# Kernel optimization log

Hardware: AMD Instinct MI355X
Metric: run time of the kernel (lower is better)

## Reference

```python
import jax, jax.numpy as jnp
import numpy as np

NUM_HEADS = 16
D_MODEL = 1024
D_K = D_MODEL // NUM_HEADS


def setup_inputs() -> dict:
    key = jax.random.key(0)
    ks = jax.random.split(key, 11)
    B, S = 2, 2048
    s = 1.0 / np.sqrt(D_MODEL)
    return {
        "Q": jax.random.normal(ks[0], (B, S, D_MODEL), jnp.float32),
        "K": jax.random.normal(ks[1], (B, S, D_MODEL), jnp.float32),
        "V": jax.random.normal(ks[2], (B, S, D_MODEL), jnp.float32),
        "Wq": jax.random.normal(ks[3], (D_MODEL, D_MODEL), jnp.float32) * s,
        "bq": jnp.zeros((D_MODEL,), jnp.float32),
        "Wk": jax.random.normal(ks[4], (D_MODEL, D_MODEL), jnp.float32) * s,
        "bk": jnp.zeros((D_MODEL,), jnp.float32),
        "Wv": jax.random.normal(ks[5], (D_MODEL, D_MODEL), jnp.float32) * s,
        "bv": jnp.zeros((D_MODEL,), jnp.float32),
        "Wo": jax.random.normal(ks[6], (D_MODEL, D_MODEL), jnp.float32) * s,
        "bo": jnp.zeros((D_MODEL,), jnp.float32),
    }


def _split_heads(x):
    B, S, _ = x.shape
    return x.reshape(B, S, NUM_HEADS, D_K).transpose(0, 2, 1, 3)  # (B,H,S,Dk)


def reference(Q, K, V, Wq, bq, Wk, bk, Wv, bv, Wo, bo):
    q = _split_heads(Q @ Wq + bq)
    k = _split_heads(K @ Wk + bk)
    v = _split_heads(V @ Wv + bv)
    scores = jnp.einsum("bhqd,bhkd->bhqk", q, k) / jnp.sqrt(jnp.asarray(D_K, q.dtype))
    attn = jax.nn.softmax(scores, axis=-1)
    out = jnp.einsum("bhqk,bhkd->bhqd", attn, v)  # (B,H,S,Dk)
    B, H, S, Dk = out.shape
    combined = out.transpose(0, 2, 1, 3).reshape(B, S, H * Dk)
    return combined @ Wo + bo
```

## Files before the change

### kernel.cpp

```cpp
#include <hip/hip_runtime.h>
#include <stdint.h>

#define DM   1024
#define NH   16
#define DKH  64
#define SEQ  2048
#define NB   2

typedef __attribute__((ext_vector_type(8))) short  frag8;
typedef __attribute__((ext_vector_type(4))) short  frag4;
typedef __attribute__((ext_vector_type(4))) short  short4v;
typedef __attribute__((ext_vector_type(8))) short  short8v;
typedef __attribute__((ext_vector_type(4))) float  f32x4;

__device__ __forceinline__ unsigned short f2bf(float x){
  unsigned u = __float_as_uint(x);
  u += 0x7fffu + ((u >> 16) & 1u);
  return (unsigned short)(u >> 16);
}

__device__ __forceinline__ float dev_exp2(float x){
  return __builtin_amdgcn_exp2f(x);
}

#define GLOAD16(GP, LP) __builtin_amdgcn_global_load_lds( \
    (__attribute__((address_space(1))) void*)(GP), \
    (__attribute__((address_space(3))) void*)(LP), 16, 0, 0)

#define LDSFENCE() do{ asm volatile("" ::: "memory"); \
                       __builtin_amdgcn_sched_barrier(0); }while(0)



__global__ __launch_bounds__(256) void cast_qkv(const float* __restrict__ Q,
                                                const float* __restrict__ K,
                                                const float* __restrict__ V,
                                                short* __restrict__ dst){
  const int z = blockIdx.z;
  const float* src = (z == 0) ? Q : (z == 1 ? K : V);
  const int i = (blockIdx.x * 256 + threadIdx.x) * 4;
  float4 f = *(const float4*)(src + i);
  short4v s;
  s.x = (short)f2bf(f.x); s.y = (short)f2bf(f.y);
  s.z = (short)f2bf(f.z); s.w = (short)f2bf(f.w);
  *(short4v*)(dst + (long)z * (SEQ*NB*DM) + i) = s;
}

__global__ __launch_bounds__(256) void wtrans(const float* __restrict__ Wq,
                                              const float* __restrict__ Wk,
                                              const float* __restrict__ Wv,
                                              const float* __restrict__ Wo,
                                              short* __restrict__ wt){
  const int z = blockIdx.z;
  const float* W = (z == 0) ? Wq : (z == 1 ? Wk : (z == 2 ? Wv : Wo));
  short* out = wt + (long)z * (DM*DM);
  __shared__ float t[32][33];
  const int n0 = blockIdx.x * 32, k0 = blockIdx.y * 32;
  const int c = threadIdx.x & 31, r0 = threadIdx.x >> 5;
#pragma unroll
  for (int i = 0; i < 4; ++i){
    int r = r0 + i * 8;
    t[r][c] = W[(k0 + r) * DM + n0 + c];
  }
  __syncthreads();
#pragma unroll
  for (int i = 0; i < 4; ++i){
    int r = r0 + i * 8;
    out[(n0 + r) * DM + k0 + c] = (short)f2bf(t[c][r]);
  }
}

__device__ __forceinline__ void store_out(short* p, float v){ *p = (short)f2bf(v); }
__device__ __forceinline__ void store_out(float* p, float v){ *p = v; }

template<typename OT>
__global__ __launch_bounds__(256) void gemm_bt(const short* __restrict__ Abase, long Astride,
                                               const short* __restrict__ Btbase, long Btstride,
                                               const float* __restrict__ bias0,
                                               const float* __restrict__ bias1,
                                               const float* __restrict__ bias2,
                                               OT* __restrict__ Cbase, long Cstride,
                                               float qscale){
  const int z = blockIdx.z;
  const short* A  = Abase + (long)z * Astride;
  const short* Bt = Btbase + (long)z * Btstride;
  OT* C = Cbase + (long)z * Cstride;
  const float* bias = (z == 0) ? bias0 : (z == 1 ? bias1 : bias2);
  const float scale = (z == 0) ? qscale : 1.0f;
  const int KD = DM, ND = DM;

  __shared__ __align__(16) short As[2][128 * 64];
  __shared__ __align__(16) short Bs[2][128 * 64];

  const int tid = threadIdx.x;
  const int w = tid >> 6, lane = tid & 63, l15 = lane & 15, quad = lane >> 4;
  const int wy = w >> 1, wx = w & 1;
  const int bm = blockIdx.x * 128, bn = blockIdx.y * 128;
  const int lrow = lane >> 3;
  const int lcolsw = (((lane & 7) ^ lrow) & 7) * 8;

  f32x4 acc[4][4] = {};

#define GSTAGE(KT, BSEL) do{                                                    \
  _Pragma("unroll")                                                             \
  for (int i_ = 0; i_ < 4; ++i_){                                               \
    int j_ = w * 4 + i_;                                                        \
    GLOAD16(A  + (bm + j_ * 8 + lrow) * KD + (KT) * 64 + lcolsw,                \
            &As[BSEL][j_ * 512]);                                               \
    GLOAD16(Bt + (bn + j_ * 8 + lrow) * KD + (KT) * 64 + lcolsw,                \
            &Bs[BSEL][j_ * 512]);                                               \
  } }while(0)

#define GCOMPUTE(BS) do{                                                        \
  _Pragma("unroll") for (int ks = 0; ks < 2; ++ks){                             \
    frag8 af[4], bf_[4];                                                        \
    _Pragma("unroll") for (int mt = 0; mt < 4; ++mt)                            \
      af[mt] = *(const frag8*)&As[BS][(wy * 64 + mt * 16 + l15) * 64 +          \
                                      (((ks * 4 + quad) ^ (l15 & 7)) * 8)];     \
    _Pragma("unroll") for (int nt = 0; nt < 4; ++nt)                            \
      bf_[nt] = *(const frag8*)&Bs[BS][(wx * 64 + nt * 16 + l15) * 64 +         \
                                       (((ks * 4 + quad) ^ (l15 & 7)) * 8)];    \
    _Pragma("unroll") for (int mt = 0; mt < 4; ++mt)                            \
      _Pragma("unroll") for (int nt = 0; nt < 4; ++nt)                          \
        acc[mt][nt] = __builtin_amdgcn_mfma_f32_16x16x32_bf16(                  \
            af[mt], bf_[nt], acc[mt][nt], 0, 0, 0);                             \
  } }while(0)

  GSTAGE(0, 0);
  for (int t = 0; t < KD / 64 - 1; ++t){
    GSTAGE(t + 1, (t + 1) & 1);
    asm volatile("s_waitcnt vmcnt(8)" ::: "memory");
    __builtin_amdgcn_s_barrier();
    LDSFENCE();
    GCOMPUTE(t & 1);
    asm volatile("s_waitcnt lgkmcnt(0)" ::: "memory");
    __builtin_amdgcn_sched_barrier(0);
    __builtin_amdgcn_s_barrier();
  }
  asm volatile("s_waitcnt vmcnt(0)" ::: "memory");
  __builtin_amdgcn_s_barrier();
  LDSFENCE();
  GCOMPUTE(1);

#undef GSTAGE
#undef GCOMPUTE

#pragma unroll
  for (int mt = 0; mt < 4; ++mt){
#pragma unroll
    for (int r = 0; r < 4; ++r){
      int m = bm + wy * 64 + mt * 16 + quad * 4 + r;
#pragma unroll
      for (int nt = 0; nt < 4; ++nt){
        int n = bn + wx * 64 + nt * 16 + l15;
        float v = (acc[mt][nt][r] + bias[n]) * scale;
        store_out(&C[(long)m * ND + n], v);
      }
    }
  }
}

template<typename OT>
__global__ __launch_bounds__(256) void gemm64_bt(const short* __restrict__ A,
                                                 const short* __restrict__ Bt,
                                                 const float* __restrict__ bias,
                                                 OT* __restrict__ C,
                                                 float scale){
  const int KD = DM, ND = DM;
  __shared__ __align__(16) short As[2][64 * 64];
  __shared__ __align__(16) short Bs[2][128 * 64];
  const int tid = threadIdx.x;
  const int w = tid >> 6, lane = tid & 63, l15 = lane & 15, quad = lane >> 4;
  const int wy = w >> 1, wx = w & 1;
  const int bm = blockIdx.x * 64, bn = blockIdx.y * 128;
  const int lrow = lane >> 3;
  const int lcolsw = (((lane & 7) ^ lrow) & 7) * 8;
  f32x4 acc[2][4] = {};

#define GSTAGE64(KT, BSEL) do{                                                  \
  _Pragma("unroll")                                                             \
  for (int i_ = 0; i_ < 2; ++i_){                                               \
    int j_ = w * 2 + i_;                                                        \
    GLOAD16(A + (bm + j_ * 8 + lrow) * KD + (KT) * 64 + lcolsw,                 \
            &As[BSEL][j_ * 512]);                                               \
  }                                                                             \
  _Pragma("unroll")                                                             \
  for (int i_ = 0; i_ < 4; ++i_){                                               \
    int j_ = w * 4 + i_;                                                        \
    GLOAD16(Bt + (bn + j_ * 8 + lrow) * KD + (KT) * 64 + lcolsw,                \
            &Bs[BSEL][j_ * 512]);                                               \
  } }while(0)

#define GCOMPUTE64(BS) do{                                                      \
  _Pragma("unroll") for (int ks = 0; ks < 2; ++ks){                             \
    frag8 af[2], bf_[4];                                                        \
    _Pragma("unroll") for (int mt = 0; mt < 2; ++mt)                            \
      af[mt] = *(const frag8*)&As[BS][(wy * 32 + mt * 16 + l15) * 64 +          \
                                      (((ks * 4 + quad) ^ (l15 & 7)) * 8)];     \
    _Pragma("unroll") for (int nt = 0; nt < 4; ++nt)                            \
      bf_[nt] = *(const frag8*)&Bs[BS][(wx * 64 + nt * 16 + l15) * 64 +         \
                                       (((ks * 4 + quad) ^ (l15 & 7)) * 8)];    \
    _Pragma("unroll") for (int mt = 0; mt < 2; ++mt)                            \
      _Pragma("unroll") for (int nt = 0; nt < 4; ++nt)                          \
        acc[mt][nt] = __builtin_amdgcn_mfma_f32_16x16x32_bf16(                  \
            af[mt], bf_[nt], acc[mt][nt], 0, 0, 0);                             \
  } }while(0)

  GSTAGE64(0, 0);
  for (int t = 0; t < KD / 64 - 1; ++t){
    GSTAGE64(t + 1, (t + 1) & 1);
    asm volatile("s_waitcnt vmcnt(6)" ::: "memory");
    __builtin_amdgcn_s_barrier();
    LDSFENCE();
    GCOMPUTE64(t & 1);
    asm volatile("s_waitcnt lgkmcnt(0)" ::: "memory");
    __builtin_amdgcn_sched_barrier(0);
    __builtin_amdgcn_s_barrier();
  }
  asm volatile("s_waitcnt vmcnt(0)" ::: "memory");
  __builtin_amdgcn_s_barrier();
  LDSFENCE();
  GCOMPUTE64(1);

#undef GSTAGE64
#undef GCOMPUTE64

#pragma unroll
  for (int mt = 0; mt < 2; ++mt){
#pragma unroll
    for (int r = 0; r < 4; ++r){
      int m = bm + wy * 32 + mt * 16 + quad * 4 + r;
#pragma unroll
      for (int nt = 0; nt < 4; ++nt){
        int n = bn + wx * 64 + nt * 16 + l15;
        store_out(&C[(long)m * ND + n], (acc[mt][nt][r] + bias[n]) * scale);
      }
    }
  }
}

__global__ __launch_bounds__(256) void vtrans(const short* __restrict__ v,
                                              short* __restrict__ vt){
  const int bh = blockIdx.y;
  const int b = bh >> 4, h = bh & 15;
  const int s0 = blockIdx.x * 64;
  __shared__ short tT[64][66];
  const short* vb = v + ((long)(b * SEQ + s0)) * DM + h * DKH;
  for (int j = threadIdx.x; j < 512; j += 256){
    int row = j >> 3, off = (j & 7) * 8;
    short8v d = *(const short8v*)(vb + row * DM + off);
#pragma unroll
    for (int e = 0; e < 8; ++e) tT[off + e][row] = d[e];
  }
  __syncthreads();
  short* out = vt + (long)bh * (DKH * SEQ) + s0;
  for (int j = threadIdx.x; j < 512; j += 256){
    int dr = j >> 3, soff = (j & 7) * 8;
    short8v o;
#pragma unroll
    for (int e = 0; e < 8; ++e) o[e] = tT[dr][soff + e];
    *(short8v*)(out + dr * SEQ + soff) = o;
  }
}

__global__ __launch_bounds__(256) void flash(const short* __restrict__ q,
                                             const short* __restrict__ k,
                                             const short* __restrict__ vt,
                                             short* __restrict__ comb){
  const int bh = blockIdx.y;
  const int b = bh >> 4, h = bh & 15;
  const int q0 = blockIdx.x * 64;
  const int tid = threadIdx.x;
  const int w = tid >> 6, lane = tid & 63, l15 = lane & 15, quad = lane >> 4;

  __shared__ __align__(16) short Ks[2][64 * 64];
  __shared__ __align__(16) short Vs[2][64 * 64];

  frag8 aq[2];
  const short* qb = q + ((long)(b * SEQ + q0 + w * 16)) * DM + h * DKH;
#pragma unroll
  for (int ks = 0; ks < 2; ++ks)
    aq[ks] = *(const frag8*)(qb + l15 * DM + ks * 32 + quad * 8);

  frag8 ones8;
#pragma unroll
  for (int e = 0; e < 8; ++e) ones8[e] = (short)0x3F80;

  f32x4 O[4] = {};
  f32x4 Lacc = {0.f, 0.f, 0.f, 0.f};

  const short* kb  = k + ((long)b * SEQ) * DM + h * DKH;
  const short* vtb = vt + (long)bh * (DKH * SEQ);
  const int lrow8 = lane >> 3;
  const int lcolsw = (((lane & 7) ^ lrow8) & 7) * 8;

#define STAGE(KT, BSEL) do{                                                     \
  _Pragma("unroll")                                                             \
  for (int i_ = 0; i_ < 2; ++i_){                                               \
    int jj_ = w * 2 + i_;                                                       \
    int kr_ = 32 * (jj_ >> 2) + 8 * ((jj_ * 2 + (lrow8 >> 2)) & 3)              \
            + 4 * ((jj_ >> 1) & 1) + (lrow8 & 3);                               \
    GLOAD16(kb  + ((KT) * 64 + kr_) * DM + lcolsw,        &Ks[BSEL][jj_ * 512]);\
    GLOAD16(vtb + (jj_ * 8 + lrow8) * SEQ + (KT) * 64 + lcolsw,                 \
            &Vs[BSEL][jj_ * 512]);                                              \
  } }while(0)

#define COMPUTE(BS) do{                                                         \
  __builtin_amdgcn_s_setprio(1);                                                \
  f32x4 scT[4];                                                                 \
  _Pragma("unroll") for (int nt = 0; nt < 4; ++nt)                              \
    scT[nt] = (f32x4){0.f, 0.f, 0.f, 0.f};                                      \
  _Pragma("unroll") for (int ks = 0; ks < 2; ++ks){                             \
    _Pragma("unroll") for (int nt = 0; nt < 4; ++nt){                           \
      frag8 ak = *(const frag8*)&Ks[BS][(nt * 16 + l15) * 64 +                  \
                                        (((ks * 4 + quad) ^ (l15 & 7)) * 8)];   \
      scT[nt] = __builtin_amdgcn_mfma_f32_16x16x32_bf16(                        \
          ak, aq[ks], scT[nt], 0, 0, 0);                                        \
    }                                                                           \
  }                                                                             \
  frag8 ap8[2];                                                                 \
  _Pragma("unroll") for (int c2 = 0; c2 < 2; ++c2){                             \
    frag8 p8;                                                                   \
    _Pragma("unroll") for (int hf = 0; hf < 2; ++hf)                            \
      _Pragma("unroll") for (int r = 0; r < 4; ++r){                            \
        float e = dev_exp2(scT[2 * c2 + hf][r]);                                \
        p8[hf * 4 + r] = (short)((__float_as_uint(e) + 0x8000u) >> 16);         \
      }                                                                         \
    ap8[c2] = p8;                                                               \
  }                                                                             \
  _Pragma("unroll") for (int c2 = 0; c2 < 2; ++c2){                             \
    _Pragma("unroll") for (int dt = 0; dt < 4; ++dt){                           \
      frag8 bv8 = *(const frag8*)&Vs[BS][(dt * 16 + l15) * 64 +                 \
                                         (((c2 * 4 + quad) ^ (l15 & 7)) * 8)];  \
      O[dt] = __builtin_amdgcn_mfma_f32_16x16x32_bf16(                          \
          ap8[c2], bv8, O[dt], 0, 0, 0);                                        \
    }                                                                           \
    Lacc = __builtin_amdgcn_mfma_f32_16x16x32_bf16(                             \
        ap8[c2], ones8, Lacc, 0, 0, 0);                                         \
  }                                                                             \
  __builtin_amdgcn_s_setprio(0);                                                \
}while(0)

  STAGE(0, 0);
  for (int t = 0; t < SEQ / 64 - 1; ++t){
    STAGE(t + 1, (t + 1) & 1);
    asm volatile("s_waitcnt vmcnt(4)" ::: "memory");
    __builtin_amdgcn_s_barrier();
    LDSFENCE();
    COMPUTE(t & 1);
    asm volatile("s_waitcnt lgkmcnt(0)" ::: "memory");
    __builtin_amdgcn_sched_barrier(0);
    __builtin_amdgcn_s_barrier();
  }
  asm volatile("s_waitcnt vmcnt(0)" ::: "memory");
  __builtin_amdgcn_s_barrier();
  LDSFENCE();
  COMPUTE(1);

#undef COMPUTE
#undef STAGE

  short* ob = comb + ((long)(b * SEQ + q0 + w * 16)) * DM + h * DKH;
#pragma unroll
  for (int r = 0; r < 4; ++r){
    float inv = 1.f / Lacc[r];
#pragma unroll
    for (int dt = 0; dt < 4; ++dt)
      ob[(quad * 4 + r) * DM + dt * 16 + l15] = (short)f2bf(O[dt][r] * inv);
  }
}

extern "C" void kernel_launch(void* const* d_in, const int* in_sizes, int n_in,
                              void* d_out, int out_size, void* d_ws, size_t ws_size,
                              hipStream_t stream){
  const float* Q  = (const float*)d_in[0];
  const float* K  = (const float*)d_in[1];
  const float* V  = (const float*)d_in[2];
  const float* Wq = (const float*)d_in[3];
  const float* bq = (const float*)d_in[4];
  const float* Wk = (const float*)d_in[5];
  const float* bk = (const float*)d_in[6];
  const float* Wv = (const float*)d_in[7];
  const float* bv = (const float*)d_in[8];
  const float* Wo = (const float*)d_in[9];
  const float* bo = (const float*)d_in[10];
  float* out = (float*)d_out;

  const long TEN = (long)NB * SEQ * DM;
  const long WEL = (long)DM * DM;
  short* ws   = (short*)d_ws;
  short* xc   = ws;
  short* wt   = xc + 3 * TEN;
  short* qkv  = wt + 4 * WEL;
  short* vtr  = qkv + 3 * TEN;
  short* comb = vtr + TEN;

  cast_qkv<<<dim3(4096, 1, 3), 256, 0, stream>>>(Q, K, V, xc);
  wtrans<<<dim3(32, 32, 4), 256, 0, stream>>>(Wq, Wk, Wv, Wo, wt);
  gemm_bt<short><<<dim3(32, 8, 3), 256, 0, stream>>>(xc, TEN, wt, WEL, bq, bk, bv,
                                                     qkv, TEN, 0.125f * 1.44269504f);
  vtrans<<<dim3(32, 32), 256, 0, stream>>>(qkv + 2 * TEN, vtr);
  flash<<<dim3(32, 32), 256, 0, stream>>>(qkv, qkv + TEN, vtr, comb);
  gemm64_bt<float><<<dim3(64, 8), 256, 0, stream>>>(comb, wt + 3 * WEL, bo, out, 1.0f);
  (void)in_sizes; (void)n_in; (void)out_size; (void)ws_size;
}
```

Measured before the change: 230.6 us.

## Use 128-query flash blocks with 8 waves and triple-buffered K/V tiles

Each flash attention block now covers 128 queries with 512 threads (8 waves) instead of 64 queries with 4 waves. Each K/V tile loaded into shared memory is therefore reused by twice as many query rows, and each thread issues one staging load pair per tile instead of two. The K/V ring grows from two to three buffers and prefetches two tiles ahead, with an unrolled-by-3 loop and a two-tile tail to hide global latency. The cost is more shared memory and registers per block, half as many blocks in the grid, and larger barriers across 8 waves.

```diff
diff --git a/kernel.cpp b/kernel.cpp
--- a/kernel.cpp
+++ b/kernel.cpp
@@ -263,18 +263,18 @@
   }
 }
 
-__global__ __launch_bounds__(256) void flash(const short* __restrict__ q,
+__global__ __launch_bounds__(512) void flash(const short* __restrict__ q,
                                              const short* __restrict__ k,
                                              const short* __restrict__ vt,
                                              short* __restrict__ comb){
   const int bh = blockIdx.y;
   const int b = bh >> 4, h = bh & 15;
-  const int q0 = blockIdx.x * 64;
+  const int q0 = blockIdx.x * 128;
   const int tid = threadIdx.x;
   const int w = tid >> 6, lane = tid & 63, l15 = lane & 15, quad = lane >> 4;
 
-  __shared__ __align__(16) short Ks[2][64 * 64];
-  __shared__ __align__(16) short Vs[2][64 * 64];
+  __shared__ __align__(16) short Ks[3][64 * 64];
+  __shared__ __align__(16) short Vs[3][64 * 64];
 
   frag8 aq[2];
   const short* qb = q + ((long)(b * SEQ + q0 + w * 16)) * DM + h * DKH;
@@ -295,15 +295,13 @@
   const int lcolsw = (((lane & 7) ^ lrow8) & 7) * 8;
 
 #define STAGE(KT, BSEL) do{                                                     \
-  _Pragma("unroll")                                                             \
-  for (int i_ = 0; i_ < 2; ++i_){                                               \
-    int jj_ = w * 2 + i_;                                                       \
-    int kr_ = 32 * (jj_ >> 2) + 8 * ((jj_ * 2 + (lrow8 >> 2)) & 3)              \
-            + 4 * ((jj_ >> 1) & 1) + (lrow8 & 3);                               \
-    GLOAD16(kb  + ((KT) * 64 + kr_) * DM + lcolsw,        &Ks[BSEL][jj_ * 512]);\
-    GLOAD16(vtb + (jj_ * 8 + lrow8) * SEQ + (KT) * 64 + lcolsw,                 \
-            &Vs[BSEL][jj_ * 512]);                                              \
-  } }while(0)
+  int jj_ = w;                                                                  \
+  int kr_ = 32 * (jj_ >> 2) + 8 * ((jj_ * 2 + (lrow8 >> 2)) & 3)                \
+          + 4 * ((jj_ >> 1) & 1) + (lrow8 & 3);                                 \
+  GLOAD16(kb  + ((KT) * 64 + kr_) * DM + lcolsw,        &Ks[BSEL][jj_ * 512]);  \
+  GLOAD16(vtb + (jj_ * 8 + lrow8) * SEQ + (KT) * 64 + lcolsw,                   \
+          &Vs[BSEL][jj_ * 512]);                                                \
+}while(0)
 
 #define COMPUTE(BS) do{                                                         \
   __builtin_amdgcn_s_setprio(1);                                                \
@@ -341,22 +339,34 @@
   __builtin_amdgcn_s_setprio(0);                                                \
 }while(0)
 
+#define ITER(KT, BC, BSNEXT) do{                                                \
+  STAGE((KT) + 2, BSNEXT);                                                      \
+  asm volatile("s_waitcnt vmcnt(4)" ::: "memory");                              \
+  __builtin_amdgcn_s_barrier();                                                 \
+  LDSFENCE();                                                                   \
+  COMPUTE(BC);                                                                  \
+  asm volatile("s_waitcnt lgkmcnt(0)" ::: "memory");                            \
+  __builtin_amdgcn_sched_barrier(0);                                            \
+  __builtin_amdgcn_s_barrier();                                                 \
+}while(0)
+
   STAGE(0, 0);
-  for (int t = 0; t < SEQ / 64 - 1; ++t){
-    STAGE(t + 1, (t + 1) & 1);
-    asm volatile("s_waitcnt vmcnt(4)" ::: "memory");
-    __builtin_amdgcn_s_barrier();
-    LDSFENCE();
-    COMPUTE(t & 1);
-    asm volatile("s_waitcnt lgkmcnt(0)" ::: "memory");
-    __builtin_amdgcn_sched_barrier(0);
-    __builtin_amdgcn_s_barrier();
-  }
+  STAGE(1, 1);
+  for (int kt = 0; kt < SEQ / 64 - 2; kt += 3){
+    ITER(kt,     0, 2);
+    ITER(kt + 1, 1, 0);
+    ITER(kt + 2, 2, 1);
+  }
+  asm volatile("s_waitcnt vmcnt(2)" ::: "memory");
+  __builtin_amdgcn_s_barrier();
+  LDSFENCE();
+  COMPUTE(0);
   asm volatile("s_waitcnt vmcnt(0)" ::: "memory");
   __builtin_amdgcn_s_barrier();
   LDSFENCE();
   COMPUTE(1);
 
+#undef ITER
 #undef COMPUTE
 #undef STAGE
 
@@ -400,7 +410,7 @@
   gemm_bt<short><<<dim3(32, 8, 3), 256, 0, stream>>>(xc, TEN, wt, WEL, bq, bk, bv,
                                                      qkv, TEN, 0.125f * 1.44269504f);
   vtrans<<<dim3(32, 32), 256, 0, stream>>>(qkv + 2 * TEN, vtr);
-  flash<<<dim3(32, 32), 256, 0, stream>>>(qkv, qkv + TEN, vtr, comb);
+  flash<<<dim3(16, 32), 512, 0, stream>>>(qkv, qkv + TEN, vtr, comb);
   gemm64_bt<float><<<dim3(64, 8), 256, 0, stream>>>(comb, wt + 3 * WEL, bo, out, 1.0f);
   (void)in_sizes; (void)n_in; (void)out_size; (void)ws_size;
 }
```

Result: faster. 222.0 us (-3.7%).
